# Kernel optimization log

Measured on AMD Instinct MI355X. Metric: run time of the kernel, lower is better.

Reference implementation:

```python
import jax, jax.numpy as jnp
import numpy as np

N_NODES = 100000
N_EDGES = 3200000


def gcn_conv(x, edge_index, W, b, num_nodes):
    """PyG GCNConv: x' = D^{-1/2} (A + I) D^{-1/2} (x W) + b (symmetric norm, self-loops)."""
    x = x @ W  # [N, out]
    loop = jnp.arange(num_nodes, dtype=edge_index.dtype)
    src = jnp.concatenate([edge_index[0], loop])
    dst = jnp.concatenate([edge_index[1], loop])
    # degree over destination nodes (incl. self loops)
    deg = jax.ops.segment_sum(jnp.ones_like(dst, dtype=x.dtype), dst, num_segments=num_nodes)
    dinv = jnp.where(deg > 0, jax.lax.rsqrt(deg), 0.0)
    norm = dinv[src] * dinv[dst]  # [E + N]
    msg = x[src] * norm[:, None]  # gather + scale
    out = jax.ops.segment_sum(msg, dst, num_segments=num_nodes)  # scatter-add
    return out + b


def setup_inputs() -> dict:
    key = jax.random.key(0)
    k = jax.random.split(key, 5)
    x = jax.random.normal(k[0], (N_NODES, 256), dtype=jnp.float32)
    edge_index = jax.random.randint(k[1], (2, N_EDGES), 0, N_NODES, dtype=jnp.int64)
    W1 = jax.random.normal(k[2], (256, 16), dtype=jnp.float32) * (1.0 / np.sqrt(256))
    b1 = jnp.zeros((16,), dtype=jnp.float32)
    W2 = jax.random.normal(k[3], (16, 8), dtype=jnp.float32) * (1.0 / np.sqrt(16))
    b2 = jnp.zeros((8,), dtype=jnp.float32)
    return {"x": x, "edge_index": edge_index, "W1": W1, "b1": b1, "W2": W2, "b2": b2}


def reference(x, edge_index, W1, b1, W2, b2):
    n = x.shape[0]
    h = gcn_conv(x, edge_index, W1, b1, n)
    h = jax.nn.relu(h)
    # dropout is identity in eval mode (training=False)
    h = gcn_conv(h, edge_index, W2, b2, n)
    return jax.nn.log_softmax(h, axis=1)
```

## Files before the change

### kernel.cpp

```cpp
#include <hip/hip_runtime.h>

#define NN 100000
#define NE 3200000
#define NB 391
#define CAP 9216
#define PB 16
#define CH_A (256 * PB)

typedef _Float16 half4 __attribute__((ext_vector_type(4)));
typedef _Float16 half8 __attribute__((ext_vector_type(8)));

__device__ __forceinline__ float4 f4fma(float s, float4 a, float4 c) {
  c.x = fmaf(s, a.x, c.x); c.y = fmaf(s, a.y, c.y);
  c.z = fmaf(s, a.z, c.z); c.w = fmaf(s, a.w, c.w);
  return c;
}

template<int CTRL>
__device__ __forceinline__ float4 quad_bcast(float4 v) {
  float4 r;
  r.x = __int_as_float(__builtin_amdgcn_update_dpp(__float_as_int(v.x), __float_as_int(v.x), CTRL, 0xF, 0xF, false));
  r.y = __int_as_float(__builtin_amdgcn_update_dpp(__float_as_int(v.y), __float_as_int(v.y), CTRL, 0xF, 0xF, false));
  r.z = __int_as_float(__builtin_amdgcn_update_dpp(__float_as_int(v.z), __float_as_int(v.z), CTRL, 0xF, 0xF, false));
  r.w = __int_as_float(__builtin_amdgcn_update_dpp(__float_as_int(v.w), __float_as_int(v.w), CTRL, 0xF, 0xF, false));
  return r;
}

__global__ __launch_bounds__(512) void init_kernel(int* __restrict__ bucket_cursor) {
  int t = threadIdx.x;
  if (t < NB) bucket_cursor[t] = 0;
}

__global__ __launch_bounds__(256) void bin_kernel(const int* __restrict__ ei,
                                                  int* __restrict__ bucket_cursor,
                                                  int* __restrict__ pairs) {
  __shared__ int  cnt[4][NB];
  __shared__ int  wcur[4][NB];
  __shared__ int  lbase[NB];
  __shared__ int  gbase[NB];
  __shared__ int  sc[512];
  __shared__ int2 stage[CH_A];
  __shared__ int  w64flag;
  int t = threadIdx.x;
  int wv = t >> 6;
  for (int k = t; k < 4 * NB; k += 256) (&cnt[0][0])[k] = 0;
  if (t < 64) {
    int o = (t < 32) ? ei[2 * t + 1] : 0;
    unsigned long long bl = __ballot(o != 0);
    if (t == 0) w64flag = (bl == 0ULL) ? 1 : 0;
  }
  __syncthreads();
  bool w64 = (w64flag != 0);
  int base = blockIdx.x * CH_A;
  int nval = min(CH_A, NE - base);
  int s[PB], d[PB];
  if (w64) {
#pragma unroll
    for (int i = 0; i < 8; ++i) {
      int e0 = base + i * 512 + 2 * t;
      if (e0 < NE) {
        int4 svv = *(const int4*)(ei + 2 * (size_t)e0);
        int4 dvv = *(const int4*)(ei + 2 * (size_t)NE + 2 * (size_t)e0);
        s[2 * i] = svv.x; s[2 * i + 1] = svv.z;
        d[2 * i] = dvv.x; d[2 * i + 1] = dvv.z;
        atomicAdd(&cnt[wv][dvv.x >> 8], 1);
        atomicAdd(&cnt[wv][dvv.z >> 8], 1);
      } else {
        d[2 * i] = -1; d[2 * i + 1] = -1;
      }
    }
  } else {
#pragma unroll
    for (int i = 0; i < PB; ++i) {
      int e = base + i * 256 + t;
      if (e < NE) {
        s[i] = ei[e];
        d[i] = ei[NE + e];
        atomicAdd(&cnt[wv][d[i] >> 8], 1);
      } else {
        d[i] = -1;
      }
    }
  }
  __syncthreads();
  int tA = (t < NB) ? cnt[0][t] + cnt[1][t] + cnt[2][t] + cnt[3][t] : 0;
  int tB = (t + 256 < NB) ? cnt[0][t + 256] + cnt[1][t + 256] + cnt[2][t + 256] + cnt[3][t + 256] : 0;
  sc[t] = tA; sc[t + 256] = tB;
  __syncthreads();
#pragma unroll
  for (int off = 1; off < 512; off <<= 1) {
    int u0 = (t >= off) ? sc[t - off] : 0;
    int u1 = (t + 256 >= off) ? sc[t + 256 - off] : 0;
    __syncthreads();
    sc[t] += u0; sc[t + 256] += u1;
    __syncthreads();
  }
#pragma unroll
  for (int h = 0; h < 2; ++h) {
    int k = t + h * 256;
    if (k < NB) {
      int tot = (h == 0) ? tA : tB;
      int lb = sc[k] - tot;
      lbase[k] = lb;
      gbase[k] = (tot > 0) ? atomicAdd(&bucket_cursor[k], tot) : 0;
      int c0 = cnt[0][k], c1 = cnt[1][k], c2 = cnt[2][k];
      wcur[0][k] = lb;
      wcur[1][k] = lb + c0;
      wcur[2][k] = lb + c0 + c1;
      wcur[3][k] = lb + c0 + c1 + c2;
    }
  }
  __syncthreads();
#pragma unroll
  for (int i = 0; i < PB; ++i) {
    if (d[i] >= 0) {
      int b = d[i] >> 8;
      int slot = atomicAdd(&wcur[wv][b], 1);
      stage[slot] = make_int2(s[i], d[i]);
    }
  }
  __syncthreads();
  for (int k = t; k < nval; k += 256) {
    int2 p = stage[k];
    int b = p.y >> 8;
    pairs[(size_t)b * CAP + gbase[b] + (k - lbase[b])] = p.x | ((p.y & 255) << 24);
  }
}

__global__ __launch_bounds__(512) void sort_kernel(const int* __restrict__ pairs,
                                                   const int* __restrict__ bucket_cursor,
                                                   int* __restrict__ srt,
                                                   int* __restrict__ deg,
                                                   int* __restrict__ row_ofs,
                                                   float* __restrict__ dinv) {
  __shared__ int hist[2][256];
  __shared__ int sc[256];
  __shared__ int cur[256];
  __shared__ int wsum[8];
  __shared__ int obase;
  int t = threadIdx.x;
  int b = blockIdx.x;
  int cnt_b = bucket_cursor[b];
  size_t in_base = (size_t)b * CAP;
  if (t < 256) { hist[0][t] = 0; hist[1][t] = 0; }
  int v = (t < b) ? bucket_cursor[t] : 0;
#pragma unroll
  for (int m = 1; m <= 32; m <<= 1) v += __shfl_xor(v, m);
  if ((t & 63) == 0) wsum[t >> 6] = v;
  __syncthreads();
  if (t == 0) {
    int s0 = 0;
#pragma unroll
    for (int k = 0; k < 8; ++k) s0 += wsum[k];
    obase = s0;
  }
  int hsel = t >> 8;
  for (int i = t; i < cnt_b; i += 512) {
    int pk = pairs[in_base + i];
    atomicAdd(&hist[hsel][((unsigned)pk) >> 24], 1);
  }
  __syncthreads();
  int out_base = obase;
  if (t < 256) sc[t] = hist[0][t] + hist[1][t];
  __syncthreads();
#pragma unroll
  for (int off = 1; off < 256; off <<= 1) {
    int u = (t < 256 && t >= off) ? sc[t - off] : 0;
    __syncthreads();
    if (t < 256) sc[t] += u;
    __syncthreads();
  }
  if (t < 256) {
    int tot = hist[0][t] + hist[1][t];
    int excl = sc[t] - tot;
    cur[t] = out_base + excl;
    int n = b * 256 + t;
    if (n < NN) {
      deg[n] = tot;
      row_ofs[n] = out_base + excl;
      dinv[n] = rsqrtf((float)tot + 1.0f);
    }
  }
  __syncthreads();
  for (int i = t; i < cnt_b; i += 512) {
    int pk = pairs[in_base + i];
    int pos = atomicAdd(&cur[((unsigned)pk) >> 24], 1);
    srt[pos] = pk & 0xFFFFFF;
  }
}

__global__ __launch_bounds__(256) void gemm1_kernel(const float* __restrict__ x,
                                                    const float* __restrict__ W1,
                                                    const float* __restrict__ dinv,
                                                    _Float16* __restrict__ xw1h) {
  const int lane = threadIdx.x & 63;
  const int wv   = threadIdx.x >> 6;
  const int node0 = (blockIdx.x * 4 + wv) * 8;
  const int cg = lane >> 2;
  const int jl = lane & 3;
  float4 w[16];
#pragma unroll
  for (int k = 0; k < 4; ++k)
#pragma unroll
    for (int c = 0; c < 4; ++c)
      w[k * 4 + c] = *(const float4*)(W1 + (cg * 16 + k * 4 + c) * 16 + jl * 4);
  float4 xv[8];
#pragma unroll
  for (int i = 0; i < 8; ++i)
    xv[i] = *(const float4*)(x + (size_t)(node0 + i) * 256 + lane * 4);
  float4 acc[8];
#pragma unroll
  for (int i = 0; i < 8; ++i) acc[i] = make_float4(0.f, 0.f, 0.f, 0.f);
#pragma unroll
  for (int i = 0; i < 8; ++i) {
    float4 b = quad_bcast<0x00>(xv[i]);
    acc[i] = f4fma(b.x, w[0], acc[i]);  acc[i] = f4fma(b.y, w[1], acc[i]);
    acc[i] = f4fma(b.z, w[2], acc[i]);  acc[i] = f4fma(b.w, w[3], acc[i]);
  }
#pragma unroll
  for (int i = 0; i < 8; ++i) {
    float4 b = quad_bcast<0x55>(xv[i]);
    acc[i] = f4fma(b.x, w[4], acc[i]);  acc[i] = f4fma(b.y, w[5], acc[i]);
    acc[i] = f4fma(b.z, w[6], acc[i]);  acc[i] = f4fma(b.w, w[7], acc[i]);
  }
#pragma unroll
  for (int i = 0; i < 8; ++i) {
    float4 b = quad_bcast<0xAA>(xv[i]);
    acc[i] = f4fma(b.x, w[8], acc[i]);  acc[i] = f4fma(b.y, w[9], acc[i]);
    acc[i] = f4fma(b.z, w[10], acc[i]); acc[i] = f4fma(b.w, w[11], acc[i]);
  }
#pragma unroll
  for (int i = 0; i < 8; ++i) {
    float4 b = quad_bcast<0xFF>(xv[i]);
    acc[i] = f4fma(b.x, w[12], acc[i]); acc[i] = f4fma(b.y, w[13], acc[i]);
    acc[i] = f4fma(b.z, w[14], acc[i]); acc[i] = f4fma(b.w, w[15], acc[i]);
  }
#pragma unroll
  for (int m = 4; m <= 32; m <<= 1) {
#pragma unroll
    for (int i = 0; i < 8; ++i) {
      acc[i].x += __shfl_xor(acc[i].x, m);
      acc[i].y += __shfl_xor(acc[i].y, m);
      acc[i].z += __shfl_xor(acc[i].z, m);
      acc[i].w += __shfl_xor(acc[i].w, m);
    }
  }
  if (lane < 4) {
#pragma unroll
    for (int i = 0; i < 8; ++i) {
      float dn = dinv[node0 + i];
      float4 a = acc[i];
      half4 hv;
      hv[0] = (_Float16)(a.x * dn); hv[1] = (_Float16)(a.y * dn);
      hv[2] = (_Float16)(a.z * dn); hv[3] = (_Float16)(a.w * dn);
      *(half4*)(xw1h + (size_t)(node0 + i) * 16 + lane * 4) = hv;
    }
  }
}

__global__ __launch_bounds__(256) void layer1_kernel(const int* __restrict__ srt,
                                                     const int* __restrict__ row_ofs,
                                                     const int* __restrict__ deg,
                                                     const float* __restrict__ dinv,
                                                     const _Float16* __restrict__ xw1h,
                                                     const float* __restrict__ W2,
                                                     const float* __restrict__ b1,
                                                     _Float16* __restrict__ h1w2h) {
  int t = blockIdx.x * 256 + threadIdx.x;
  int n = t >> 3, sub = t & 7, q = sub & 1, e = sub >> 1;
  if (n >= NN) return;
  int base = row_ofs[n], cnt = deg[n];
  float acc[8] = {0.f, 0.f, 0.f, 0.f, 0.f, 0.f, 0.f, 0.f};
  int s_next = (e < cnt) ? srt[base + e] : 0;
  for (int i = e; i < cnt; i += 4) {
    int s = s_next;
    if (i + 4 < cnt) s_next = srt[base + i + 4];
    half8 v = *(const half8*)(xw1h + (size_t)s * 16 + q * 8);
#pragma unroll
    for (int j = 0; j < 8; ++j) acc[j] += (float)v[j];
  }
#pragma unroll
  for (int m = 2; m <= 4; m <<= 1)
#pragma unroll
    for (int j = 0; j < 8; ++j) acc[j] += __shfl_xor(acc[j], m);
  float dn = dinv[n];
  half8 sv = *(const half8*)(xw1h + (size_t)n * 16 + q * 8);
  float bb[8];
  *(float4*)bb       = *(const float4*)(b1 + q * 8);
  *(float4*)(bb + 4) = *(const float4*)(b1 + q * 8 + 4);
  float h[8];
#pragma unroll
  for (int j = 0; j < 8; ++j)
    h[j] = fmaxf(fmaf(dn, acc[j] + (float)sv[j], bb[j]), 0.f);
  float p[8] = {0.f, 0.f, 0.f, 0.f, 0.f, 0.f, 0.f, 0.f};
  const float4* W2v = (const float4*)W2;
#pragma unroll
  for (int f = 0; f < 8; ++f) {
    float4 wlo = W2v[(q * 8 + f) * 2];
    float4 whi = W2v[(q * 8 + f) * 2 + 1];
    p[0] = fmaf(h[f], wlo.x, p[0]); p[1] = fmaf(h[f], wlo.y, p[1]);
    p[2] = fmaf(h[f], wlo.z, p[2]); p[3] = fmaf(h[f], wlo.w, p[3]);
    p[4] = fmaf(h[f], whi.x, p[4]); p[5] = fmaf(h[f], whi.y, p[5]);
    p[6] = fmaf(h[f], whi.z, p[6]); p[7] = fmaf(h[f], whi.w, p[7]);
  }
#pragma unroll
  for (int j = 0; j < 8; ++j) p[j] += __shfl_xor(p[j], 1);
  if (sub == 0) {
    half8 hv;
#pragma unroll
    for (int j = 0; j < 8; ++j) hv[j] = (_Float16)(p[j] * dn);
    *(half8*)(h1w2h + (size_t)n * 8) = hv;
  }
}

__global__ __launch_bounds__(256) void layer2_kernel(const int* __restrict__ srt,
                                                     const int* __restrict__ row_ofs,
                                                     const int* __restrict__ deg,
                                                     const float* __restrict__ dinv,
                                                     const _Float16* __restrict__ h1w2h,
                                                     const float* __restrict__ b2,
                                                     float* __restrict__ out) {
  int t = blockIdx.x * 256 + threadIdx.x;
  int n = t >> 2, e = t & 3;
  if (n >= NN) return;
  int base = row_ofs[n], cnt = deg[n];
  float acc[8] = {0.f, 0.f, 0.f, 0.f, 0.f, 0.f, 0.f, 0.f};
  int s_next = (e < cnt) ? srt[base + e] : 0;
  for (int i = e; i < cnt; i += 4) {
    int s = s_next;
    if (i + 4 < cnt) s_next = srt[base + i + 4];
    half8 v = *(const half8*)(h1w2h + (size_t)s * 8);
#pragma unroll
    for (int j = 0; j < 8; ++j) acc[j] += (float)v[j];
  }
#pragma unroll
  for (int m = 1; m <= 2; m <<= 1)
#pragma unroll
    for (int j = 0; j < 8; ++j) acc[j] += __shfl_xor(acc[j], m);
  float dn = dinv[n];
  half8 sv = *(const half8*)(h1w2h + (size_t)n * 8);
  float bb[8];
  *(float4*)bb       = *(const float4*)b2;
  *(float4*)(bb + 4) = *(const float4*)(b2 + 4);
  float v8[8];
#pragma unroll
  for (int j = 0; j < 8; ++j) v8[j] = fmaf(dn, acc[j] + (float)sv[j], bb[j]);
  float mx = v8[0];
#pragma unroll
  for (int j = 1; j < 8; ++j) mx = fmaxf(mx, v8[j]);
  float se = 0.f;
#pragma unroll
  for (int j = 0; j < 8; ++j) se += expf(v8[j] - mx);
  float ls = mx + logf(se);
  if (e < 2) {
    float4 o4 = (e == 0)
        ? make_float4(v8[0] - ls, v8[1] - ls, v8[2] - ls, v8[3] - ls)
        : make_float4(v8[4] - ls, v8[5] - ls, v8[6] - ls, v8[7] - ls);
    *(float4*)(out + (size_t)n * 8 + e * 4) = o4;
  }
}

extern "C" void kernel_launch(void* const* d_in, const int* in_sizes, int n_in,
                              void* d_out, int out_size, void* d_ws, size_t ws_size,
                              hipStream_t stream) {
  const float* x  = (const float*)d_in[0];
  const int*   ei = (const int*)d_in[1];
  const float* W1 = (const float*)d_in[2];
  const float* b1 = (const float*)d_in[3];
  const float* W2 = (const float*)d_in[4];
  const float* b2 = (const float*)d_in[5];
  float* out = (float*)d_out;

  int*      pairs = (int*)d_ws;
  _Float16* xw1h  = (_Float16*)(pairs + (size_t)NB * CAP);
  _Float16* h1w2h = xw1h + (size_t)16 * NN;
  float*    dinv  = (float*)(h1w2h + (size_t)8 * NN);
  int*      deg   = (int*)(dinv + NN);
  int*      row_ofs = deg + NN;
  int*      srt   = row_ofs + NN;
  int*      bucket_cursor = srt + NE;

  init_kernel<<<1, 512, 0, stream>>>(bucket_cursor);
  bin_kernel<<<(NE + CH_A - 1) / CH_A, 256, 0, stream>>>(ei, bucket_cursor, pairs);
  sort_kernel<<<NB, 512, 0, stream>>>(pairs, bucket_cursor, srt, deg, row_ofs, dinv);
  gemm1_kernel<<<NN / 32, 256, 0, stream>>>(x, W1, dinv, xw1h);
  layer1_kernel<<<(8 * NN + 255) / 256, 256, 0, stream>>>(srt, row_ofs, deg, dinv, xw1h, W2, b1, h1w2h);
  layer2_kernel<<<(4 * NN + 255) / 256, 256, 0, stream>>>(srt, row_ofs, deg, dinv, h1w2h, b2, out);
}
```

Before: 306.3 us.

## Drop per-bucket sort; aggregate bucketed edges via shared-memory atomics

Removes the sort kernel and the CSR (srt/row_ofs) build. Degrees are now counted with global atomics in the bin kernel, and dinv is computed on the fly with rsqrt. Both aggregation layers become one 1024-thread block per 256-node bucket that scatters gathered features into shared-memory accumulators with atomic adds. This saves a full pass over the edges and one launch, but adds heavy LDS atomic traffic, only 391 blocks, and nondeterministic float summation order.

```diff
diff --git a/kernel.cpp b/kernel.cpp
--- a/kernel.cpp
+++ b/kernel.cpp
@@ -26,14 +26,10 @@
   return r;
 }
 
-__global__ __launch_bounds__(512) void init_kernel(int* __restrict__ bucket_cursor) {
-  int t = threadIdx.x;
-  if (t < NB) bucket_cursor[t] = 0;
-}
-
 __global__ __launch_bounds__(256) void bin_kernel(const int* __restrict__ ei,
                                                   int* __restrict__ bucket_cursor,
-                                                  int* __restrict__ pairs) {
+                                                  int* __restrict__ pairs,
+                                                  int* __restrict__ deg) {
   __shared__ int  cnt[4][NB];
   __shared__ int  wcur[4][NB];
   __shared__ int  lbase[NB];
@@ -124,74 +120,13 @@
     int2 p = stage[k];
     int b = p.y >> 8;
     pairs[(size_t)b * CAP + gbase[b] + (k - lbase[b])] = p.x | ((p.y & 255) << 24);
-  }
-}
-
-__global__ __launch_bounds__(512) void sort_kernel(const int* __restrict__ pairs,
-                                                   const int* __restrict__ bucket_cursor,
-                                                   int* __restrict__ srt,
-                                                   int* __restrict__ deg,
-                                                   int* __restrict__ row_ofs,
-                                                   float* __restrict__ dinv) {
-  __shared__ int hist[2][256];
-  __shared__ int sc[256];
-  __shared__ int cur[256];
-  __shared__ int wsum[8];
-  __shared__ int obase;
-  int t = threadIdx.x;
-  int b = blockIdx.x;
-  int cnt_b = bucket_cursor[b];
-  size_t in_base = (size_t)b * CAP;
-  if (t < 256) { hist[0][t] = 0; hist[1][t] = 0; }
-  int v = (t < b) ? bucket_cursor[t] : 0;
-#pragma unroll
-  for (int m = 1; m <= 32; m <<= 1) v += __shfl_xor(v, m);
-  if ((t & 63) == 0) wsum[t >> 6] = v;
-  __syncthreads();
-  if (t == 0) {
-    int s0 = 0;
-#pragma unroll
-    for (int k = 0; k < 8; ++k) s0 += wsum[k];
-    obase = s0;
-  }
-  int hsel = t >> 8;
-  for (int i = t; i < cnt_b; i += 512) {
-    int pk = pairs[in_base + i];
-    atomicAdd(&hist[hsel][((unsigned)pk) >> 24], 1);
-  }
-  __syncthreads();
-  int out_base = obase;
-  if (t < 256) sc[t] = hist[0][t] + hist[1][t];
-  __syncthreads();
-#pragma unroll
-  for (int off = 1; off < 256; off <<= 1) {
-    int u = (t < 256 && t >= off) ? sc[t - off] : 0;
-    __syncthreads();
-    if (t < 256) sc[t] += u;
-    __syncthreads();
-  }
-  if (t < 256) {
-    int tot = hist[0][t] + hist[1][t];
-    int excl = sc[t] - tot;
-    cur[t] = out_base + excl;
-    int n = b * 256 + t;
-    if (n < NN) {
-      deg[n] = tot;
-      row_ofs[n] = out_base + excl;
-      dinv[n] = rsqrtf((float)tot + 1.0f);
-    }
-  }
-  __syncthreads();
-  for (int i = t; i < cnt_b; i += 512) {
-    int pk = pairs[in_base + i];
-    int pos = atomicAdd(&cur[((unsigned)pk) >> 24], 1);
-    srt[pos] = pk & 0xFFFFFF;
+    atomicAdd(&deg[p.y], 1);
   }
 }
 
 __global__ __launch_bounds__(256) void gemm1_kernel(const float* __restrict__ x,
                                                     const float* __restrict__ W1,
-                                                    const float* __restrict__ dinv,
+                                                    const int* __restrict__ deg,
                                                     _Float16* __restrict__ xw1h) {
   const int lane = threadIdx.x & 63;
   const int wv   = threadIdx.x >> 6;
@@ -248,7 +183,7 @@
   if (lane < 4) {
 #pragma unroll
     for (int i = 0; i < 8; ++i) {
-      float dn = dinv[node0 + i];
+      float dn = rsqrtf((float)deg[node0 + i] + 1.0f);
       float4 a = acc[i];
       half4 hv;
       hv[0] = (_Float16)(a.x * dn); hv[1] = (_Float16)(a.y * dn);
@@ -258,105 +193,124 @@
   }
 }
 
-__global__ __launch_bounds__(256) void layer1_kernel(const int* __restrict__ srt,
-                                                     const int* __restrict__ row_ofs,
-                                                     const int* __restrict__ deg,
-                                                     const float* __restrict__ dinv,
-                                                     const _Float16* __restrict__ xw1h,
-                                                     const float* __restrict__ W2,
-                                                     const float* __restrict__ b1,
-                                                     _Float16* __restrict__ h1w2h) {
-  int t = blockIdx.x * 256 + threadIdx.x;
-  int n = t >> 3, sub = t & 7, q = sub & 1, e = sub >> 1;
-  if (n >= NN) return;
-  int base = row_ofs[n], cnt = deg[n];
-  float acc[8] = {0.f, 0.f, 0.f, 0.f, 0.f, 0.f, 0.f, 0.f};
-  int s_next = (e < cnt) ? srt[base + e] : 0;
-  for (int i = e; i < cnt; i += 4) {
-    int s = s_next;
-    if (i + 4 < cnt) s_next = srt[base + i + 4];
-    half8 v = *(const half8*)(xw1h + (size_t)s * 16 + q * 8);
-#pragma unroll
-    for (int j = 0; j < 8; ++j) acc[j] += (float)v[j];
-  }
-#pragma unroll
-  for (int m = 2; m <= 4; m <<= 1)
-#pragma unroll
-    for (int j = 0; j < 8; ++j) acc[j] += __shfl_xor(acc[j], m);
-  float dn = dinv[n];
-  half8 sv = *(const half8*)(xw1h + (size_t)n * 16 + q * 8);
-  float bb[8];
-  *(float4*)bb       = *(const float4*)(b1 + q * 8);
-  *(float4*)(bb + 4) = *(const float4*)(b1 + q * 8 + 4);
-  float h[8];
-#pragma unroll
-  for (int j = 0; j < 8; ++j)
-    h[j] = fmaxf(fmaf(dn, acc[j] + (float)sv[j], bb[j]), 0.f);
-  float p[8] = {0.f, 0.f, 0.f, 0.f, 0.f, 0.f, 0.f, 0.f};
-  const float4* W2v = (const float4*)W2;
-#pragma unroll
-  for (int f = 0; f < 8; ++f) {
-    float4 wlo = W2v[(q * 8 + f) * 2];
-    float4 whi = W2v[(q * 8 + f) * 2 + 1];
-    p[0] = fmaf(h[f], wlo.x, p[0]); p[1] = fmaf(h[f], wlo.y, p[1]);
-    p[2] = fmaf(h[f], wlo.z, p[2]); p[3] = fmaf(h[f], wlo.w, p[3]);
-    p[4] = fmaf(h[f], whi.x, p[4]); p[5] = fmaf(h[f], whi.y, p[5]);
-    p[6] = fmaf(h[f], whi.z, p[6]); p[7] = fmaf(h[f], whi.w, p[7]);
-  }
-#pragma unroll
-  for (int j = 0; j < 8; ++j) p[j] += __shfl_xor(p[j], 1);
-  if (sub == 0) {
-    half8 hv;
-#pragma unroll
-    for (int j = 0; j < 8; ++j) hv[j] = (_Float16)(p[j] * dn);
-    *(half8*)(h1w2h + (size_t)n * 8) = hv;
-  }
-}
-
-__global__ __launch_bounds__(256) void layer2_kernel(const int* __restrict__ srt,
-                                                     const int* __restrict__ row_ofs,
-                                                     const int* __restrict__ deg,
-                                                     const float* __restrict__ dinv,
-                                                     const _Float16* __restrict__ h1w2h,
-                                                     const float* __restrict__ b2,
-                                                     float* __restrict__ out) {
-  int t = blockIdx.x * 256 + threadIdx.x;
-  int n = t >> 2, e = t & 3;
-  if (n >= NN) return;
-  int base = row_ofs[n], cnt = deg[n];
-  float acc[8] = {0.f, 0.f, 0.f, 0.f, 0.f, 0.f, 0.f, 0.f};
-  int s_next = (e < cnt) ? srt[base + e] : 0;
-  for (int i = e; i < cnt; i += 4) {
-    int s = s_next;
-    if (i + 4 < cnt) s_next = srt[base + i + 4];
+__global__ __launch_bounds__(1024) void agg1_kernel(const int* __restrict__ pairs,
+                                                    const int* __restrict__ bucket_cursor,
+                                                    const int* __restrict__ deg,
+                                                    const _Float16* __restrict__ xw1h,
+                                                    const float* __restrict__ W2,
+                                                    const float* __restrict__ b1,
+                                                    _Float16* __restrict__ h1w2h) {
+  __shared__ float acc[16][257];
+  int t = threadIdx.x;
+  int b = blockIdx.x;
+  int cnt_b = bucket_cursor[b];
+  size_t in_base = (size_t)b * CAP;
+  for (int k = t; k < 16 * 257; k += 1024) (&acc[0][0])[k] = 0.f;
+  __syncthreads();
+  for (int i = t; i < cnt_b; i += 1024) {
+    int pk = pairs[in_base + i];
+    int s  = pk & 0xFFFFFF;
+    int nl = ((unsigned)pk) >> 24;
+    half8 v0 = *(const half8*)(xw1h + (size_t)s * 16);
+    half8 v1 = *(const half8*)(xw1h + (size_t)s * 16 + 8);
+    atomicAdd(&acc[0][nl],  (float)v0[0]);
+    atomicAdd(&acc[1][nl],  (float)v0[1]);
+    atomicAdd(&acc[2][nl],  (float)v0[2]);
+    atomicAdd(&acc[3][nl],  (float)v0[3]);
+    atomicAdd(&acc[4][nl],  (float)v0[4]);
+    atomicAdd(&acc[5][nl],  (float)v0[5]);
+    atomicAdd(&acc[6][nl],  (float)v0[6]);
+    atomicAdd(&acc[7][nl],  (float)v0[7]);
+    atomicAdd(&acc[8][nl],  (float)v1[0]);
+    atomicAdd(&acc[9][nl],  (float)v1[1]);
+    atomicAdd(&acc[10][nl], (float)v1[2]);
+    atomicAdd(&acc[11][nl], (float)v1[3]);
+    atomicAdd(&acc[12][nl], (float)v1[4]);
+    atomicAdd(&acc[13][nl], (float)v1[5]);
+    atomicAdd(&acc[14][nl], (float)v1[6]);
+    atomicAdd(&acc[15][nl], (float)v1[7]);
+  }
+  __syncthreads();
+  int n0 = t >> 2, sub = t & 3;
+  int n = b * 256 + n0;
+  if (n < NN) {
+    float dn = rsqrtf((float)deg[n] + 1.0f);
+    half4 sv = *(const half4*)(xw1h + (size_t)n * 16 + sub * 4);
+    float4 bv = *(const float4*)(b1 + sub * 4);
+    float bb[4] = {bv.x, bv.y, bv.z, bv.w};
+    float p[8] = {0.f, 0.f, 0.f, 0.f, 0.f, 0.f, 0.f, 0.f};
+    const float4* W2v = (const float4*)W2;
+#pragma unroll
+    for (int f = 0; f < 4; ++f) {
+      int fg = sub * 4 + f;
+      float h = fmaxf(fmaf(dn, acc[fg][n0] + (float)sv[f], bb[f]), 0.f);
+      float4 wlo = W2v[fg * 2];
+      float4 whi = W2v[fg * 2 + 1];
+      p[0] = fmaf(h, wlo.x, p[0]); p[1] = fmaf(h, wlo.y, p[1]);
+      p[2] = fmaf(h, wlo.z, p[2]); p[3] = fmaf(h, wlo.w, p[3]);
+      p[4] = fmaf(h, whi.x, p[4]); p[5] = fmaf(h, whi.y, p[5]);
+      p[6] = fmaf(h, whi.z, p[6]); p[7] = fmaf(h, whi.w, p[7]);
+    }
+#pragma unroll
+    for (int m = 1; m <= 2; m <<= 1)
+#pragma unroll
+      for (int j = 0; j < 8; ++j)
+        p[j] += __shfl_xor(p[j], m);
+    if (sub == 0) {
+      half8 hv;
+#pragma unroll
+      for (int j = 0; j < 8; ++j) hv[j] = (_Float16)(p[j] * dn);
+      *(half8*)(h1w2h + (size_t)n * 8) = hv;
+    }
+  }
+}
+
+__global__ __launch_bounds__(1024) void agg2_kernel(const int* __restrict__ pairs,
+                                                    const int* __restrict__ bucket_cursor,
+                                                    const int* __restrict__ deg,
+                                                    const _Float16* __restrict__ h1w2h,
+                                                    const float* __restrict__ b2,
+                                                    float* __restrict__ out) {
+  __shared__ float acc[8][257];
+  int t = threadIdx.x;
+  int b = blockIdx.x;
+  int cnt_b = bucket_cursor[b];
+  size_t in_base = (size_t)b * CAP;
+  for (int k = t; k < 8 * 257; k += 1024) (&acc[0][0])[k] = 0.f;
+  __syncthreads();
+  for (int i = t; i < cnt_b; i += 1024) {
+    int pk = pairs[in_base + i];
+    int s  = pk & 0xFFFFFF;
+    int nl = ((unsigned)pk) >> 24;
     half8 v = *(const half8*)(h1w2h + (size_t)s * 8);
-#pragma unroll
-    for (int j = 0; j < 8; ++j) acc[j] += (float)v[j];
-  }
-#pragma unroll
-  for (int m = 1; m <= 2; m <<= 1)
-#pragma unroll
-    for (int j = 0; j < 8; ++j) acc[j] += __shfl_xor(acc[j], m);
-  float dn = dinv[n];
-  half8 sv = *(const half8*)(h1w2h + (size_t)n * 8);
-  float bb[8];
-  *(float4*)bb       = *(const float4*)b2;
-  *(float4*)(bb + 4) = *(const float4*)(b2 + 4);
-  float v8[8];
-#pragma unroll
-  for (int j = 0; j < 8; ++j) v8[j] = fmaf(dn, acc[j] + (float)sv[j], bb[j]);
-  float mx = v8[0];
-#pragma unroll
-  for (int j = 1; j < 8; ++j) mx = fmaxf(mx, v8[j]);
-  float se = 0.f;
-#pragma unroll
-  for (int j = 0; j < 8; ++j) se += expf(v8[j] - mx);
-  float ls = mx + logf(se);
-  if (e < 2) {
-    float4 o4 = (e == 0)
-        ? make_float4(v8[0] - ls, v8[1] - ls, v8[2] - ls, v8[3] - ls)
-        : make_float4(v8[4] - ls, v8[5] - ls, v8[6] - ls, v8[7] - ls);
-    *(float4*)(out + (size_t)n * 8 + e * 4) = o4;
+    atomicAdd(&acc[0][nl], (float)v[0]);
+    atomicAdd(&acc[1][nl], (float)v[1]);
+    atomicAdd(&acc[2][nl], (float)v[2]);
+    atomicAdd(&acc[3][nl], (float)v[3]);
+    atomicAdd(&acc[4][nl], (float)v[4]);
+    atomicAdd(&acc[5][nl], (float)v[5]);
+    atomicAdd(&acc[6][nl], (float)v[6]);
+    atomicAdd(&acc[7][nl], (float)v[7]);
+  }
+  __syncthreads();
+  if (t < 512) {
+    int n0 = t >> 1, q = t & 1;
+    int n = b * 256 + n0;
+    if (n < NN) {
+      float dn = rsqrtf((float)deg[n] + 1.0f);
+      half4 sv = *(const half4*)(h1w2h + (size_t)n * 8 + q * 4);
+      float4 bv = *(const float4*)(b2 + q * 4);
+      float v0 = fmaf(dn, acc[q * 4 + 0][n0] + (float)sv[0], bv.x);
+      float v1 = fmaf(dn, acc[q * 4 + 1][n0] + (float)sv[1], bv.y);
+      float v2 = fmaf(dn, acc[q * 4 + 2][n0] + (float)sv[2], bv.z);
+      float v3 = fmaf(dn, acc[q * 4 + 3][n0] + (float)sv[3], bv.w);
+      float mh = fmaxf(fmaxf(v0, v1), fmaxf(v2, v3));
+      float m = fmaxf(mh, __shfl_xor(mh, 1));
+      float se = expf(v0 - m) + expf(v1 - m) + expf(v2 - m) + expf(v3 - m);
+      float st = se + __shfl_xor(se, 1);
+      float ls = m + logf(st);
+      *(float4*)(out + (size_t)n * 8 + q * 4) = make_float4(v0 - ls, v1 - ls, v2 - ls, v3 - ls);
+    }
   }
 }
 
@@ -371,19 +325,15 @@
   const float* b2 = (const float*)d_in[5];
   float* out = (float*)d_out;
 
-  int*      pairs = (int*)d_ws;
+  int*      deg           = (int*)d_ws;
+  int*      bucket_cursor = deg + NN;
+  int*      pairs         = deg + 100392;
   _Float16* xw1h  = (_Float16*)(pairs + (size_t)NB * CAP);
   _Float16* h1w2h = xw1h + (size_t)16 * NN;
-  float*    dinv  = (float*)(h1w2h + (size_t)8 * NN);
-  int*      deg   = (int*)(dinv + NN);
-  int*      row_ofs = deg + NN;
-  int*      srt   = row_ofs + NN;
-  int*      bucket_cursor = srt + NE;
-
-  init_kernel<<<1, 512, 0, stream>>>(bucket_cursor);
-  bin_kernel<<<(NE + CH_A - 1) / CH_A, 256, 0, stream>>>(ei, bucket_cursor, pairs);
-  sort_kernel<<<NB, 512, 0, stream>>>(pairs, bucket_cursor, srt, deg, row_ofs, dinv);
-  gemm1_kernel<<<NN / 32, 256, 0, stream>>>(x, W1, dinv, xw1h);
-  layer1_kernel<<<(8 * NN + 255) / 256, 256, 0, stream>>>(srt, row_ofs, deg, dinv, xw1h, W2, b1, h1w2h);
-  layer2_kernel<<<(4 * NN + 255) / 256, 256, 0, stream>>>(srt, row_ofs, deg, dinv, h1w2h, b2, out);
-}
+
+  hipMemsetAsync(deg, 0, (size_t)(NN + NB) * sizeof(int), stream);
+  bin_kernel<<<(NE + CH_A - 1) / CH_A, 256, 0, stream>>>(ei, bucket_cursor, pairs, deg);
+  gemm1_kernel<<<NN / 32, 256, 0, stream>>>(x, W1, deg, xw1h);
+  agg1_kernel<<<NB, 1024, 0, stream>>>(pairs, bucket_cursor, deg, xw1h, W2, b1, h1w2h);
+  agg2_kernel<<<NB, 1024, 0, stream>>>(pairs, bucket_cursor, deg, h1w2h, b2, out);
+}
```

After: 837.4 us. 2.73x slower.
